# Kernel tuning notes

Hardware: AMD Instinct MI355X
Metric: run time of the kernel (lower is better)

The kernel has to match this reference:

```python
import jax, jax.numpy as jnp
import numpy as np

DIM = 192
HEADS = 6
WIN = (2, 6, 2)
N_TOK = WIN[0] * WIN[1] * WIN[2]  # 24
MLP_HID = 4 * DIM


def _rel_pos_index():
    wh, ww, wd = WIN
    ch, cw, cd = np.meshgrid(np.arange(wh), np.arange(ww), np.arange(wd), indexing='ij')
    coords = np.stack([ch, cw, cd]).reshape(3, -1)  # (3, N)
    rel = coords[:, :, None] - coords[:, None, :]   # (3, N, N)
    rel = rel.transpose(1, 2, 0).copy()
    rel[:, :, 0] += wh - 1
    rel[:, :, 1] += ww - 1
    rel[:, :, 2] += wd - 1
    rel[:, :, 0] *= (2 * ww - 1) * (2 * wd - 1)
    rel[:, :, 1] *= 2 * wd - 1
    return rel.sum(-1)  # (N, N) int


def setup_inputs() -> dict:
    key = jax.random.key(0)
    ks = jax.random.split(key, 8)
    wh, ww, wd = WIN
    table_len = (2 * wh - 1) * (2 * ww - 1) * (2 * wd - 1)
    return {
        'x': jax.random.normal(ks[0], (2, 48, 96, 14, DIM), jnp.float32),
        'ln1_g': jnp.ones((DIM,), jnp.float32),
        'ln1_b': jnp.zeros((DIM,), jnp.float32),
        'qkv_w': jax.random.normal(ks[1], (DIM, 3 * DIM), jnp.float32) * 0.02,  # [in, out]
        'qkv_b': jnp.zeros((3 * DIM,), jnp.float32),
        'bias_table': jax.random.normal(ks[2], (table_len, HEADS), jnp.float32) * 0.02,
        'proj_w': jax.random.normal(ks[3], (DIM, DIM), jnp.float32) * 0.02,
        'proj_b': jnp.zeros((DIM,), jnp.float32),
        'ln2_g': jnp.ones((DIM,), jnp.float32),
        'ln2_b': jnp.zeros((DIM,), jnp.float32),
        'mlp_w1': jax.random.normal(ks[4], (DIM, MLP_HID), jnp.float32) * 0.02,
        'mlp_b1': jnp.zeros((MLP_HID,), jnp.float32),
        'mlp_w2': jax.random.normal(ks[5], (MLP_HID, DIM), jnp.float32) * 0.02,
        'mlp_b2': jnp.zeros((DIM,), jnp.float32),
        'rel_index': jnp.asarray(_rel_pos_index(), jnp.int32),  # (N, N)
    }


def _layernorm(x, g, b, eps=1e-5):
    mu = jnp.mean(x, -1, keepdims=True)
    var = jnp.mean(jnp.square(x - mu), -1, keepdims=True)
    return (x - mu) * jax.lax.rsqrt(var + eps) * g + b


def reference(x, ln1_g, ln1_b, qkv_w, qkv_b, bias_table, proj_w, proj_b,
              ln2_g, ln2_b, mlp_w1, mlp_b1, mlp_w2, mlp_b2, rel_index):
    B, H, W, D, C = x.shape
    wh, ww, wd = WIN
    pad_h, pad_w, pad_d = (-H) % wh, (-W) % ww, (-D) % wd
    if pad_h or pad_w or pad_d:
        x = jnp.pad(x, ((0, 0), (0, pad_h), (0, pad_w), (0, pad_d), (0, 0)))
    Hp, Wp, Dp = H + pad_h, W + pad_w, D + pad_d
    # window partition -> (num_windows*B, N, C)
    xw = x.reshape(B, Hp // wh, wh, Wp // ww, ww, Dp // wd, wd, C)
    xw = xw.transpose(0, 1, 3, 5, 2, 4, 6, 7).reshape(-1, N_TOK, C)
    shortcut = xw

    h = _layernorm(xw, ln1_g, ln1_b)
    qkv = (h @ qkv_w + qkv_b).reshape(-1, N_TOK, 3, HEADS, C // HEADS)
    q, k, v = qkv[:, :, 0], qkv[:, :, 1], qkv[:, :, 2]  # (Bw, N, H, hd)
    scale = (C // HEADS) ** -0.5
    attn = jnp.einsum('bnhd,bmhd->bhnm', q * scale, k)
    bias = bias_table[rel_index]  # (N, N, HEADS)
    attn = attn + bias.transpose(2, 0, 1)[None]
    attn = jax.nn.softmax(attn, axis=-1)
    out = jnp.einsum('bhnm,bmhd->bnhd', attn, v).reshape(-1, N_TOK, C)
    out = out @ proj_w + proj_b
    xw = shortcut + out

    h2 = _layernorm(xw, ln2_g, ln2_b)
    mlp = jax.nn.gelu(h2 @ mlp_w1 + mlp_b1, approximate=False) @ mlp_w2 + mlp_b2
    xw = xw + mlp

    # reverse window partition
    xw = xw.reshape(B, Hp // wh, Wp // ww, Dp // wd, wh, ww, wd, C)
    xw = xw.transpose(0, 1, 4, 2, 5, 3, 6, 7).reshape(B, Hp, Wp, Dp, C)
    if pad_h or pad_w or pad_d:
        xw = xw[:, :H, :W, :D, :]
    return xw
```

## Files before the change

### kernel.cpp

```cpp
#include <hip/hip_runtime.h>
#include <hip/hip_bf16.h>
#include <math.h>

typedef __bf16 bf16_t;
typedef __bf16 bf16x8 __attribute__((ext_vector_type(8)));
typedef float  f32x4  __attribute__((ext_vector_type(4)));

#define NBLK 2688
#define WP_QKV  0
#define WP_PROJ 55296
#define WP_MLP1 73728
#define WP_MLP2 147456
#define WP_TOT  221184
#define WF_QKV  0
#define WF_PROJ 110592
#define WF_MLP1 147456
#define WF_MLP2 294912

__global__ void preproc_all(const float* __restrict__ qkv_w, const float* __restrict__ proj_w,
                            const float* __restrict__ mlp_w1, const float* __restrict__ mlp_w2,
                            bf16_t* __restrict__ dst) {
    int p = blockIdx.x * 256 + threadIdx.x;
    if (p >= WP_TOT) return;
    const float* W; int N, Kt; int q = p;
    if (p < WP_PROJ)      { W = qkv_w;  N = 576; Kt = 6;  }
    else if (p < WP_MLP1) { W = proj_w; N = 192; Kt = 6;  q -= WP_PROJ; }
    else if (p < WP_MLP2) { W = mlp_w1; N = 768; Kt = 6;  q -= WP_MLP1; }
    else                  { W = mlp_w2; N = 192; Kt = 24; q -= WP_MLP2; }
    int j    = (q & 3) * 2;
    int lane = (q >> 2) & 63;
    int kt   = (q >> 8) % Kt;
    int nt   = (q >> 8) / Kt;
    int k = kt * 32 + (lane >> 4) * 8 + j;
    int n = nt * 16 + (lane & 15);
    union { bf16_t h[2]; unsigned u; } pk;
    pk.h[0] = (bf16_t)W[k * N + n];
    pk.h[1] = (bf16_t)W[(k + 1) * N + n];
    *(unsigned*)(dst + p * 2) = pk.u;
}

__global__ __launch_bounds__(384, 3)
void pangu_main(const float* __restrict__ x,
                const float* __restrict__ ln1_g, const float* __restrict__ ln1_b,
                const float* __restrict__ qkv_b,
                const float* __restrict__ bias_table,
                const float* __restrict__ proj_b,
                const float* __restrict__ ln2_g, const float* __restrict__ ln2_b,
                const float* __restrict__ mlp_b1, const float* __restrict__ mlp_b2,
                const int* __restrict__ rel_index,
                const bf16_t* __restrict__ wf,
                float* __restrict__ out)
{
    __shared__ __align__(16) unsigned char arena[115200];
    __shared__ int   sRowOff[48];
    __shared__ float sMu[48], sRs[48];

    unsigned char* aAb   = arena;
    unsigned char* aOb   = arena;
    unsigned char* aH2b  = arena;
    unsigned char* xw2b  = arena + 19200;
    unsigned char* aHidb = arena + 38400;
    bf16_t* aO   = (bf16_t*)aOb;
    bf16_t* aHid = (bf16_t*)aHidb;
    bf16_t* xw2h = (bf16_t*)xw2b;

    const int t    = threadIdx.x;
    const int lane = t & 63;
    const int wv   = t >> 6;
    const int quad = lane >> 4;
    const int l15  = lane & 15;
    const int q4   = quad * 4;

    if (t < 48) {
        int win = t / 24, tok = t % 24;
        int W = blockIdx.x * 2 + win;
        int id_ = W % 7;  int r1 = W / 7;
        int iw_ = r1 % 16; int r2 = r1 / 16;
        int ih_ = r2 % 24; int b  = r2 / 24;
        int i = tok / 12, j = (tok % 12) / 2, k = tok % 2;
        sRowOff[t] = (((b * 48 + ih_ * 2 + i) * 96 + iw_ * 6 + j) * 14 + id_ * 2 + k) * 192;
    }
    __syncthreads();

    {
        int r48 = t >> 3, l = t & 7;
        const float* xr = x + sRowOff[r48];
        float4 v[6];
        #pragma unroll
        for (int s = 0; s < 6; ++s) v[s] = *(const float4*)(xr + l * 4 + s * 32);
        float sm = 0.f, s2 = 0.f;
        #pragma unroll
        for (int s = 0; s < 6; ++s) {
            sm += v[s].x + v[s].y + v[s].z + v[s].w;
            s2 += v[s].x * v[s].x + v[s].y * v[s].y + v[s].z * v[s].z + v[s].w * v[s].w;
        }
        sm += __shfl_xor(sm, 1); s2 += __shfl_xor(s2, 1);
        sm += __shfl_xor(sm, 2); s2 += __shfl_xor(s2, 2);
        sm += __shfl_xor(sm, 4); s2 += __shfl_xor(s2, 4);
        float mu = sm * (1.f / 192.f);
        float var = s2 * (1.f / 192.f) - mu * mu;
        float rs = rsqrtf(var + 1e-5f);
        int row = r48;
        #pragma unroll
        for (int s = 0; s < 6; ++s) {
            int c = l * 4 + s * 32;
            union { bf16_t h[4]; uint2 u; } pk;
            pk.h[0] = (bf16_t)((v[s].x - mu) * rs * ln1_g[c]     + ln1_b[c]);
            pk.h[1] = (bf16_t)((v[s].y - mu) * rs * ln1_g[c + 1] + ln1_b[c + 1]);
            pk.h[2] = (bf16_t)((v[s].z - mu) * rs * ln1_g[c + 2] + ln1_b[c + 2]);
            pk.h[3] = (bf16_t)((v[s].w - mu) * rs * ln1_g[c + 3] + ln1_b[c + 3]);
            *(uint2*)(aAb + row * 400 + c * 2) = pk.u;
        }
    }
    __syncthreads();

    {
        const int h = wv;
        unsigned char* wb = arena + 19200 + wv * 9344;
        bf16_t* Qb  = (bf16_t*)wb;
        bf16_t* Kb2 = (bf16_t*)(wb + 1920);
        bf16_t* Vt  = (bf16_t*)(wb + 5760);
        bf16_t* Pb  = (bf16_t*)wb;

        {
            f32x4 acc[3][4];
            const int ntg[4] = {12+2*h, 13+2*h, 24+2*h, 25+2*h};
            float bq[4];
            #pragma unroll
            for (int n = 0; n < 4; ++n) bq[n] = qkv_b[ntg[n] * 16 + l15];
            #pragma unroll
            for (int m = 0; m < 3; ++m)
                #pragma unroll
                for (int n = 0; n < 4; ++n)
                    acc[m][n] = (f32x4){bq[n], bq[n], bq[n], bq[n]};
            for (int kt = 0; kt < 6; ++kt) {
                bf16x8 af[3];
                #pragma unroll
                for (int m = 0; m < 3; ++m)
                    af[m] = *(const bf16x8*)(aAb + (l15 + m * 16) * 400 + kt * 64 + quad * 16);
                #pragma unroll
                for (int n = 0; n < 4; ++n) {
                    bf16x8 bfr = *(const bf16x8*)(wf + WF_QKV + ((ntg[n] * 6 + kt) * 64 + lane) * 8);
                    #pragma unroll
                    for (int m = 0; m < 3; ++m)
                        acc[m][n] = __builtin_amdgcn_mfma_f32_16x16x32_bf16(af[m], bfr, acc[m][n], 0, 0, 0);
                }
            }
            #pragma unroll
            for (int m = 0; m < 3; ++m)
                #pragma unroll
                for (int i = 0; i < 4; ++i) {
                    int row = m * 16 + q4 + i;
                    #pragma unroll
                    for (int nt = 0; nt < 2; ++nt) {
                        int d = nt * 16 + l15;
                        Kb2[row * 40 + d] = (bf16_t)(acc[m][nt][i]);
                        Vt[d * 56 + row]  = (bf16_t)(acc[m][2+nt][i]);
                    }
                }
            {
                int d = lane >> 1, half = lane & 1;
                *(uint2*)((unsigned char*)Vt + d * 112 + 96 + half * 8) = make_uint2(0u, 0u);
            }
        }

        f32x4 qacc[3][2];
        {
            const int ntg[2] = {2*h, 2*h+1};
            float bq[2];
            #pragma unroll
            for (int n = 0; n < 2; ++n) bq[n] = qkv_b[ntg[n] * 16 + l15];
            #pragma unroll
            for (int m = 0; m < 3; ++m)
                #pragma unroll
                for (int n = 0; n < 2; ++n)
                    qacc[m][n] = (f32x4){bq[n], bq[n], bq[n], bq[n]};
            for (int kt = 0; kt < 6; ++kt) {
                bf16x8 af[3];
                #pragma unroll
                for (int m = 0; m < 3; ++m)
                    af[m] = *(const bf16x8*)(aAb + (l15 + m * 16) * 400 + kt * 64 + quad * 16);
                #pragma unroll
                for (int n = 0; n < 2; ++n) {
                    bf16x8 bfr = *(const bf16x8*)(wf + WF_QKV + ((ntg[n] * 6 + kt) * 64 + lane) * 8);
                    #pragma unroll
                    for (int m = 0; m < 3; ++m)
                        qacc[m][n] = __builtin_amdgcn_mfma_f32_16x16x32_bf16(af[m], bfr, qacc[m][n], 0, 0, 0);
                }
            }
        }
        __syncthreads();

        const float scale = 0.1767766952966369f;
        #pragma unroll
        for (int win = 0; win < 2; ++win) {
            #pragma unroll
            for (int m = 0; m < 3; ++m)
                #pragma unroll
                for (int i = 0; i < 4; ++i) {
                    int tok = m * 16 + q4 + i - win * 24;
                    if (tok >= 0 && tok < 24) {
                        #pragma unroll
                        for (int nt = 0; nt < 2; ++nt)
                            Qb[tok * 40 + nt * 16 + l15] = (bf16_t)(qacc[m][nt][i] * scale);
                    }
                }
            f32x4 sacc[2][2];
            #pragma unroll
            for (int mt = 0; mt < 2; ++mt)
                #pragma unroll
                for (int nt = 0; nt < 2; ++nt)
                    #pragma unroll
                    for (int i = 0; i < 4; ++i) {
                        int n = mt * 16 + q4 + i; if (n > 23) n = 23;
                        int m = nt * 16 + l15;    if (m > 23) m = 23;
                        sacc[mt][nt][i] = bias_table[rel_index[n * 24 + m] * 6 + h];
                    }
            #pragma unroll
            for (int nt = 0; nt < 2; ++nt) {
                bf16x8 kf = *(const bf16x8*)((unsigned char*)Kb2 + (win * 24 + l15 + nt * 16) * 80 + quad * 16);
                #pragma unroll
                for (int mt = 0; mt < 2; ++mt) {
                    bf16x8 qf = *(const bf16x8*)((unsigned char*)Qb + (l15 + mt * 16) * 80 + quad * 16);
                    sacc[mt][nt] = __builtin_amdgcn_mfma_f32_16x16x32_bf16(qf, kf, sacc[mt][nt], 0, 0, 0);
                }
            }
            #pragma unroll
            for (int mt = 0; mt < 2; ++mt)
                #pragma unroll
                for (int i = 0; i < 4; ++i) {
                    float s0 = sacc[mt][0][i];
                    float s1m = (l15 < 8) ? sacc[mt][1][i] : -1e30f;
                    float mx = fmaxf(s0, s1m);
                    mx = fmaxf(mx, __shfl_xor(mx, 1));
                    mx = fmaxf(mx, __shfl_xor(mx, 2));
                    mx = fmaxf(mx, __shfl_xor(mx, 4));
                    mx = fmaxf(mx, __shfl_xor(mx, 8));
                    float e0 = __expf(s0 - mx);
                    float e1 = (l15 < 8) ? __expf(sacc[mt][1][i] - mx) : 0.f;
                    float sum = e0 + e1;
                    sum += __shfl_xor(sum, 1);
                    sum += __shfl_xor(sum, 2);
                    sum += __shfl_xor(sum, 4);
                    sum += __shfl_xor(sum, 8);
                    float inv = 1.f / sum;
                    sacc[mt][0][i] = e0 * inv;
                    sacc[mt][1][i] = e1 * inv;
                }
            #pragma unroll
            for (int mt = 0; mt < 2; ++mt)
                #pragma unroll
                for (int i = 0; i < 4; ++i) {
                    int r = mt * 16 + q4 + i;
                    if (r < 24) {
                        Pb[r * 40 + l15]      = (bf16_t)sacc[mt][0][i];
                        Pb[r * 40 + 16 + l15] = (bf16_t)sacc[mt][1][i];
                    }
                }
            f32x4 oacc[2][2];
            #pragma unroll
            for (int mt = 0; mt < 2; ++mt)
                #pragma unroll
                for (int nt = 0; nt < 2; ++nt)
                    oacc[mt][nt] = (f32x4){0.f, 0.f, 0.f, 0.f};
            #pragma unroll
            for (int nt = 0; nt < 2; ++nt) {
                bf16x8 vf = *(const bf16x8*)((unsigned char*)Vt + (l15 + nt * 16) * 112 + win * 48 + quad * 16);
                #pragma unroll
                for (int mt = 0; mt < 2; ++mt) {
                    bf16x8 pf = *(const bf16x8*)((unsigned char*)Pb + (l15 + mt * 16) * 80 + quad * 16);
                    oacc[mt][nt] = __builtin_amdgcn_mfma_f32_16x16x32_bf16(pf, vf, oacc[mt][nt], 0, 0, 0);
                }
            }
            #pragma unroll
            for (int mt = 0; mt < 2; ++mt)
                #pragma unroll
                for (int i = 0; i < 4; ++i) {
                    int tok = mt * 16 + q4 + i;
                    if (tok < 24) {
                        int r = win * 24 + tok;
                        #pragma unroll
                        for (int nt = 0; nt < 2; ++nt)
                            aO[r * 200 + h * 32 + nt * 16 + l15] = (bf16_t)oacc[mt][nt][i];
                    }
                }
        }
    }
    __syncthreads();

    float rxw[3][2][4];
    {
        f32x4 pacc[3][2];
        #pragma unroll
        for (int m = 0; m < 3; ++m)
            #pragma unroll
            for (int n = 0; n < 2; ++n) pacc[m][n] = (f32x4){0.f, 0.f, 0.f, 0.f};
        for (int kt = 0; kt < 6; ++kt) {
            bf16x8 af[3];
            #pragma unroll
            for (int m = 0; m < 3; ++m)
                af[m] = *(const bf16x8*)(aOb + (l15 + m * 16) * 400 + kt * 64 + quad * 16);
            #pragma unroll
            for (int n = 0; n < 2; ++n) {
                int NT = wv * 2 + n;
                bf16x8 bfr = *(const bf16x8*)(wf + WF_PROJ + ((NT * 6 + kt) * 64 + lane) * 8);
                #pragma unroll
                for (int m = 0; m < 3; ++m)
                    pacc[m][n] = __builtin_amdgcn_mfma_f32_16x16x32_bf16(af[m], bfr, pacc[m][n], 0, 0, 0);
            }
        }
        __syncthreads();
        #pragma unroll
        for (int n = 0; n < 2; ++n) {
            int c = (wv * 2 + n) * 16 + l15;
            float pb = proj_b[c];
            #pragma unroll
            for (int m = 0; m < 3; ++m)
                #pragma unroll
                for (int i = 0; i < 4; ++i) {
                    int r = m * 16 + q4 + i;
                    float val = x[sRowOff[r] + c] + pb + pacc[m][n][i];
                    rxw[m][n][i] = val;
                    xw2h[r * 200 + c] = (bf16_t)val;
                }
        }
    }
    __syncthreads();

    {
        int r = t >> 3, l = t & 7;
        float sm = 0.f, s2 = 0.f;
        #pragma unroll
        for (int s = 0; s < 6; ++s) {
            union { bf16_t h[4]; uint2 u; } pk;
            pk.u = *(const uint2*)(xw2b + r * 400 + l * 8 + s * 64);
            #pragma unroll
            for (int z = 0; z < 4; ++z) { float v = (float)pk.h[z]; sm += v; s2 += v * v; }
        }
        sm += __shfl_xor(sm, 1); s2 += __shfl_xor(s2, 1);
        sm += __shfl_xor(sm, 2); s2 += __shfl_xor(s2, 2);
        sm += __shfl_xor(sm, 4); s2 += __shfl_xor(s2, 4);
        if (l == 0) {
            float mu = sm * (1.f / 192.f);
            float var = s2 * (1.f / 192.f) - mu * mu;
            sMu[r] = mu; sRs[r] = rsqrtf(var + 1e-5f);
        }
    }
    __syncthreads();
    for (int p = t; p < 4608; p += 384) {
        int r = p / 96, c2 = p % 96, c = c2 * 2;
        float mu = sMu[r], rs = sRs[r];
        union { bf16_t h[2]; unsigned u; } in, pk;
        in.u = *(const unsigned*)(xw2b + r * 400 + c2 * 4);
        pk.h[0] = (bf16_t)(((float)in.h[0] - mu) * rs * ln2_g[c]     + ln2_b[c]);
        pk.h[1] = (bf16_t)(((float)in.h[1] - mu) * rs * ln2_g[c + 1] + ln2_b[c + 1]);
        *(unsigned*)(aH2b + r * 400 + c2 * 4) = pk.u;
    }
    __syncthreads();

    f32x4 acc2[3][2];
    #pragma unroll
    for (int m = 0; m < 3; ++m)
        #pragma unroll
        for (int n = 0; n < 2; ++n) {
            float b2 = mlp_b2[(wv * 2 + n) * 16 + l15];
            acc2[m][n] = (f32x4){b2, b2, b2, b2};
        }
    for (int ch = 0; ch < 4; ++ch) {
        f32x4 a1[3][2];
        #pragma unroll
        for (int m = 0; m < 3; ++m)
            #pragma unroll
            for (int n = 0; n < 2; ++n) {
                float b1 = mlp_b1[ch * 192 + (wv * 2 + n) * 16 + l15];
                a1[m][n] = (f32x4){b1, b1, b1, b1};
            }
        for (int kt = 0; kt < 6; ++kt) {
            bf16x8 af[3];
            #pragma unroll
            for (int m = 0; m < 3; ++m)
                af[m] = *(const bf16x8*)(aH2b + (l15 + m * 16) * 400 + kt * 64 + quad * 16);
            #pragma unroll
            for (int n = 0; n < 2; ++n) {
                int NT = ch * 12 + wv * 2 + n;
                bf16x8 bfr = *(const bf16x8*)(wf + WF_MLP1 + ((NT * 6 + kt) * 64 + lane) * 8);
                #pragma unroll
                for (int m = 0; m < 3; ++m)
                    a1[m][n] = __builtin_amdgcn_mfma_f32_16x16x32_bf16(af[m], bfr, a1[m][n], 0, 0, 0);
            }
        }
        #pragma unroll
        for (int n = 0; n < 2; ++n) {
            int c = ch * 192 + (wv * 2 + n) * 16 + l15;
            #pragma unroll
            for (int m = 0; m < 3; ++m)
                #pragma unroll
                for (int i = 0; i < 4; ++i) {
                    int r = m * 16 + q4 + i;
                    float v = a1[m][n][i];
                    float g = 0.5f * v * (1.f + erff(v * 0.70710678118654752f));
                    aHid[r * 800 + c] = (bf16_t)g;
                }
        }
    }
    __syncthreads();
    for (int ktg = 0; ktg < 24; ++ktg) {
        bf16x8 af[3];
        #pragma unroll
        for (int m = 0; m < 3; ++m)
            af[m] = *(const bf16x8*)(aHidb + (l15 + m * 16) * 1600 + ktg * 64 + quad * 16);
        #pragma unroll
        for (int n = 0; n < 2; ++n) {
            int NT = wv * 2 + n;
            bf16x8 bfr = *(const bf16x8*)(wf + WF_MLP2 + ((NT * 24 + ktg) * 64 + lane) * 8);
            #pragma unroll
            for (int m = 0; m < 3; ++m)
                acc2[m][n] = __builtin_amdgcn_mfma_f32_16x16x32_bf16(af[m], bfr, acc2[m][n], 0, 0, 0);
        }
    }

    #pragma unroll
    for (int n = 0; n < 2; ++n) {
        int c = (wv * 2 + n) * 16 + l15;
        #pragma unroll
        for (int m = 0; m < 3; ++m)
            #pragma unroll
            for (int i = 0; i < 4; ++i) {
                int r = m * 16 + q4 + i;
                out[sRowOff[r] + c] = rxw[m][n][i] + acc2[m][n][i];
            }
    }
}

extern "C" void kernel_launch(void* const* d_in, const int* in_sizes, int n_in,
                              void* d_out, int out_size, void* d_ws, size_t ws_size,
                              hipStream_t stream) {
    const float* x          = (const float*)d_in[0];
    const float* ln1_g      = (const float*)d_in[1];
    const float* ln1_b      = (const float*)d_in[2];
    const float* qkv_w      = (const float*)d_in[3];
    const float* qkv_b      = (const float*)d_in[4];
    const float* bias_table = (const float*)d_in[5];
    const float* proj_w     = (const float*)d_in[6];
    const float* proj_b     = (const float*)d_in[7];
    const float* ln2_g      = (const float*)d_in[8];
    const float* ln2_b      = (const float*)d_in[9];
    const float* mlp_w1     = (const float*)d_in[10];
    const float* mlp_b1     = (const float*)d_in[11];
    const float* mlp_w2     = (const float*)d_in[12];
    const float* mlp_b2     = (const float*)d_in[13];
    const int*   rel_index  = (const int*)d_in[14];
    float* out = (float*)d_out;
    bf16_t* wsb = (bf16_t*)d_ws;

    preproc_all<<<(WP_TOT + 255) / 256, 256, 0, stream>>>(qkv_w, proj_w, mlp_w1, mlp_w2, wsb);

    pangu_main<<<NBLK, 384, 0, stream>>>(
        x, ln1_g, ln1_b, qkv_b, bias_table, proj_b, ln2_g, ln2_b,
        mlp_b1, mlp_b2, rel_index, wsb, out);
}
```

Baseline: 505.1 us.

## Process four windows per 768-thread block with two row groups per head

Each block now handles four windows (96 tokens) with 12 waves. Waves are paired per head, and each wave covers half the token rows, so every bf16 weight fragment fetched from global memory serves twice as many rows. The MLP hidden layer is split into two 384-wide chunks, with the second matmul accumulating after each chunk, which shrinks the hidden buffer enough for the larger tile to fit in LDS. The cost is about 152KB of shared memory per block, which allows only one block per CU, plus an extra barrier in the MLP loop.

```diff
diff --git a/kernel.cpp b/kernel.cpp
--- a/kernel.cpp
+++ b/kernel.cpp
@@ -6,7 +6,7 @@
 typedef __bf16 bf16x8 __attribute__((ext_vector_type(8)));
 typedef float  f32x4  __attribute__((ext_vector_type(4)));
 
-#define NBLK 2688
+#define NBLK 1344
 #define WP_QKV  0
 #define WP_PROJ 55296
 #define WP_MLP1 73728
@@ -39,7 +39,7 @@
     *(unsigned*)(dst + p * 2) = pk.u;
 }
 
-__global__ __launch_bounds__(384, 3)
+__global__ __launch_bounds__(768, 3)
 void pangu_main(const float* __restrict__ x,
                 const float* __restrict__ ln1_g, const float* __restrict__ ln1_b,
                 const float* __restrict__ qkv_b,
@@ -51,15 +51,15 @@
                 const bf16_t* __restrict__ wf,
                 float* __restrict__ out)
 {
-    __shared__ __align__(16) unsigned char arena[115200];
-    __shared__ int   sRowOff[48];
-    __shared__ float sMu[48], sRs[48];
+    __shared__ __align__(16) unsigned char arena[152064];
+    __shared__ int   sRowOff[96];
+    __shared__ float sMu[96], sRs[96];
 
     unsigned char* aAb   = arena;
     unsigned char* aOb   = arena;
     unsigned char* aH2b  = arena;
-    unsigned char* xw2b  = arena + 19200;
-    unsigned char* aHidb = arena + 38400;
+    unsigned char* xw2b  = arena + 38400;
+    unsigned char* aHidb = arena + 76800;
     bf16_t* aO   = (bf16_t*)aOb;
     bf16_t* aHid = (bf16_t*)aHidb;
     bf16_t* xw2h = (bf16_t*)xw2b;
@@ -67,13 +67,15 @@
     const int t    = threadIdx.x;
     const int lane = t & 63;
     const int wv   = t >> 6;
+    const int h    = wv >> 1;
+    const int g    = wv & 1;
     const int quad = lane >> 4;
     const int l15  = lane & 15;
     const int q4   = quad * 4;
 
-    if (t < 48) {
+    if (t < 96) {
         int win = t / 24, tok = t % 24;
-        int W = blockIdx.x * 2 + win;
+        int W = blockIdx.x * 4 + win;
         int id_ = W % 7;  int r1 = W / 7;
         int iw_ = r1 % 16; int r2 = r1 / 16;
         int ih_ = r2 % 24; int b  = r2 / 24;
@@ -83,8 +85,8 @@
     __syncthreads();
 
     {
-        int r48 = t >> 3, l = t & 7;
-        const float* xr = x + sRowOff[r48];
+        int r96 = t >> 3, l = t & 7;
+        const float* xr = x + sRowOff[r96];
         float4 v[6];
         #pragma unroll
         for (int s = 0; s < 6; ++s) v[s] = *(const float4*)(xr + l * 4 + s * 32);
@@ -100,23 +102,21 @@
         float mu = sm * (1.f / 192.f);
         float var = s2 * (1.f / 192.f) - mu * mu;
         float rs = rsqrtf(var + 1e-5f);
-        int row = r48;
         #pragma unroll
         for (int s = 0; s < 6; ++s) {
             int c = l * 4 + s * 32;
-            union { bf16_t h[4]; uint2 u; } pk;
-            pk.h[0] = (bf16_t)((v[s].x - mu) * rs * ln1_g[c]     + ln1_b[c]);
-            pk.h[1] = (bf16_t)((v[s].y - mu) * rs * ln1_g[c + 1] + ln1_b[c + 1]);
-            pk.h[2] = (bf16_t)((v[s].z - mu) * rs * ln1_g[c + 2] + ln1_b[c + 2]);
-            pk.h[3] = (bf16_t)((v[s].w - mu) * rs * ln1_g[c + 3] + ln1_b[c + 3]);
-            *(uint2*)(aAb + row * 400 + c * 2) = pk.u;
+            union { bf16_t h4[4]; uint2 u; } pk;
+            pk.h4[0] = (bf16_t)((v[s].x - mu) * rs * ln1_g[c]     + ln1_b[c]);
+            pk.h4[1] = (bf16_t)((v[s].y - mu) * rs * ln1_g[c + 1] + ln1_b[c + 1]);
+            pk.h4[2] = (bf16_t)((v[s].z - mu) * rs * ln1_g[c + 2] + ln1_b[c + 2]);
+            pk.h4[3] = (bf16_t)((v[s].w - mu) * rs * ln1_g[c + 3] + ln1_b[c + 3]);
+            *(uint2*)(aAb + r96 * 400 + c * 2) = pk.u;
         }
     }
     __syncthreads();
 
     {
-        const int h = wv;
-        unsigned char* wb = arena + 19200 + wv * 9344;
+        unsigned char* wb = arena + 38400 + wv * 9344;
         bf16_t* Qb  = (bf16_t*)wb;
         bf16_t* Kb2 = (bf16_t*)(wb + 1920);
         bf16_t* Vt  = (bf16_t*)(wb + 5760);
@@ -137,7 +137,7 @@
                 bf16x8 af[3];
                 #pragma unroll
                 for (int m = 0; m < 3; ++m)
-                    af[m] = *(const bf16x8*)(aAb + (l15 + m * 16) * 400 + kt * 64 + quad * 16);
+                    af[m] = *(const bf16x8*)(aAb + (l15 + (3*g + m) * 16) * 400 + kt * 64 + quad * 16);
                 #pragma unroll
                 for (int n = 0; n < 4; ++n) {
                     bf16x8 bfr = *(const bf16x8*)(wf + WF_QKV + ((ntg[n] * 6 + kt) * 64 + lane) * 8);
@@ -179,7 +179,7 @@
                 bf16x8 af[3];
                 #pragma unroll
                 for (int m = 0; m < 3; ++m)
-                    af[m] = *(const bf16x8*)(aAb + (l15 + m * 16) * 400 + kt * 64 + quad * 16);
+                    af[m] = *(const bf16x8*)(aAb + (l15 + (3*g + m) * 16) * 400 + kt * 64 + quad * 16);
                 #pragma unroll
                 for (int n = 0; n < 2; ++n) {
                     bf16x8 bfr = *(const bf16x8*)(wf + WF_QKV + ((ntg[n] * 6 + kt) * 64 + lane) * 8);
@@ -193,12 +193,12 @@
 
         const float scale = 0.1767766952966369f;
         #pragma unroll
-        for (int win = 0; win < 2; ++win) {
-            #pragma unroll
-            for (int m = 0; m < 3; ++m)
-                #pragma unroll
-                for (int i = 0; i < 4; ++i) {
-                    int tok = m * 16 + q4 + i - win * 24;
+        for (int w01 = 0; w01 < 2; ++w01) {
+            #pragma unroll
+            for (int m = 0; m < 3; ++m)
+                #pragma unroll
+                for (int i = 0; i < 4; ++i) {
+                    int tok = m * 16 + q4 + i - w01 * 24;
                     if (tok >= 0 && tok < 24) {
                         #pragma unroll
                         for (int nt = 0; nt < 2; ++nt)
@@ -218,7 +218,7 @@
                     }
             #pragma unroll
             for (int nt = 0; nt < 2; ++nt) {
-                bf16x8 kf = *(const bf16x8*)((unsigned char*)Kb2 + (win * 24 + l15 + nt * 16) * 80 + quad * 16);
+                bf16x8 kf = *(const bf16x8*)((unsigned char*)Kb2 + (w01 * 24 + l15 + nt * 16) * 80 + quad * 16);
                 #pragma unroll
                 for (int mt = 0; mt < 2; ++mt) {
                     bf16x8 qf = *(const bf16x8*)((unsigned char*)Qb + (l15 + mt * 16) * 80 + quad * 16);
@@ -265,7 +265,7 @@
                     oacc[mt][nt] = (f32x4){0.f, 0.f, 0.f, 0.f};
             #pragma unroll
             for (int nt = 0; nt < 2; ++nt) {
-                bf16x8 vf = *(const bf16x8*)((unsigned char*)Vt + (l15 + nt * 16) * 112 + win * 48 + quad * 16);
+                bf16x8 vf = *(const bf16x8*)((unsigned char*)Vt + (l15 + nt * 16) * 112 + w01 * 48 + quad * 16);
                 #pragma unroll
                 for (int mt = 0; mt < 2; ++mt) {
                     bf16x8 pf = *(const bf16x8*)((unsigned char*)Pb + (l15 + mt * 16) * 80 + quad * 16);
@@ -278,7 +278,7 @@
                 for (int i = 0; i < 4; ++i) {
                     int tok = mt * 16 + q4 + i;
                     if (tok < 24) {
-                        int r = win * 24 + tok;
+                        int r = 48 * g + w01 * 24 + tok;
                         #pragma unroll
                         for (int nt = 0; nt < 2; ++nt)
                             aO[r * 200 + h * 32 + nt * 16 + l15] = (bf16_t)oacc[mt][nt][i];
@@ -299,26 +299,25 @@
             bf16x8 af[3];
             #pragma unroll
             for (int m = 0; m < 3; ++m)
-                af[m] = *(const bf16x8*)(aOb + (l15 + m * 16) * 400 + kt * 64 + quad * 16);
+                af[m] = *(const bf16x8*)(aOb + (l15 + (3*g + m) * 16) * 400 + kt * 64 + quad * 16);
             #pragma unroll
             for (int n = 0; n < 2; ++n) {
-                int NT = wv * 2 + n;
+                int NT = 2 * h + n;
                 bf16x8 bfr = *(const bf16x8*)(wf + WF_PROJ + ((NT * 6 + kt) * 64 + lane) * 8);
                 #pragma unroll
                 for (int m = 0; m < 3; ++m)
                     pacc[m][n] = __builtin_amdgcn_mfma_f32_16x16x32_bf16(af[m], bfr, pacc[m][n], 0, 0, 0);
             }
         }
-        __syncthreads();
         #pragma unroll
         for (int n = 0; n < 2; ++n) {
-            int c = (wv * 2 + n) * 16 + l15;
+            int c = (2 * h + n) * 16 + l15;
             float pb = proj_b[c];
             #pragma unroll
             for (int m = 0; m < 3; ++m)
                 #pragma unroll
                 for (int i = 0; i < 4; ++i) {
-                    int r = m * 16 + q4 + i;
+                    int r = (3*g + m) * 16 + q4 + i;
                     float val = x[sRowOff[r] + c] + pb + pacc[m][n][i];
                     rxw[m][n][i] = val;
                     xw2h[r * 200 + c] = (bf16_t)val;
@@ -332,10 +331,10 @@
         float sm = 0.f, s2 = 0.f;
         #pragma unroll
         for (int s = 0; s < 6; ++s) {
-            union { bf16_t h[4]; uint2 u; } pk;
+            union { bf16_t h4[4]; uint2 u; } pk;
             pk.u = *(const uint2*)(xw2b + r * 400 + l * 8 + s * 64);
             #pragma unroll
-            for (int z = 0; z < 4; ++z) { float v = (float)pk.h[z]; sm += v; s2 += v * v; }
+            for (int z = 0; z < 4; ++z) { float v = (float)pk.h4[z]; sm += v; s2 += v * v; }
         }
         sm += __shfl_xor(sm, 1); s2 += __shfl_xor(s2, 1);
         sm += __shfl_xor(sm, 2); s2 += __shfl_xor(s2, 2);
@@ -347,13 +346,13 @@
         }
     }
     __syncthreads();
-    for (int p = t; p < 4608; p += 384) {
+    for (int p = t; p < 9216; p += 768) {
         int r = p / 96, c2 = p % 96, c = c2 * 2;
         float mu = sMu[r], rs = sRs[r];
-        union { bf16_t h[2]; unsigned u; } in, pk;
+        union { bf16_t h2[2]; unsigned u; } in, pk;
         in.u = *(const unsigned*)(xw2b + r * 400 + c2 * 4);
-        pk.h[0] = (bf16_t)(((float)in.h[0] - mu) * rs * ln2_g[c]     + ln2_b[c]);
-        pk.h[1] = (bf16_t)(((float)in.h[1] - mu) * rs * ln2_g[c + 1] + ln2_b[c + 1]);
+        pk.h2[0] = (bf16_t)(((float)in.h2[0] - mu) * rs * ln2_g[c]     + ln2_b[c]);
+        pk.h2[1] = (bf16_t)(((float)in.h2[1] - mu) * rs * ln2_g[c + 1] + ln2_b[c + 1]);
         *(unsigned*)(aH2b + r * 400 + c2 * 4) = pk.u;
     }
     __syncthreads();
@@ -363,26 +362,26 @@
     for (int m = 0; m < 3; ++m)
         #pragma unroll
         for (int n = 0; n < 2; ++n) {
-            float b2 = mlp_b2[(wv * 2 + n) * 16 + l15];
+            float b2 = mlp_b2[(2 * h + n) * 16 + l15];
             acc2[m][n] = (f32x4){b2, b2, b2, b2};
         }
-    for (int ch = 0; ch < 4; ++ch) {
-        f32x4 a1[3][2];
+    for (int ch = 0; ch < 2; ++ch) {
+        f32x4 a1[3][4];
         #pragma unroll
         for (int m = 0; m < 3; ++m)
             #pragma unroll
-            for (int n = 0; n < 2; ++n) {
-                float b1 = mlp_b1[ch * 192 + (wv * 2 + n) * 16 + l15];
+            for (int n = 0; n < 4; ++n) {
+                float b1 = mlp_b1[(ch * 24 + 4 * h + n) * 16 + l15];
                 a1[m][n] = (f32x4){b1, b1, b1, b1};
             }
         for (int kt = 0; kt < 6; ++kt) {
             bf16x8 af[3];
             #pragma unroll
             for (int m = 0; m < 3; ++m)
-                af[m] = *(const bf16x8*)(aH2b + (l15 + m * 16) * 400 + kt * 64 + quad * 16);
-            #pragma unroll
-            for (int n = 0; n < 2; ++n) {
-                int NT = ch * 12 + wv * 2 + n;
+                af[m] = *(const bf16x8*)(aH2b + (l15 + (3*g + m) * 16) * 400 + kt * 64 + quad * 16);
+            #pragma unroll
+            for (int n = 0; n < 4; ++n) {
+                int NT = ch * 24 + 4 * h + n;
                 bf16x8 bfr = *(const bf16x8*)(wf + WF_MLP1 + ((NT * 6 + kt) * 64 + lane) * 8);
                 #pragma unroll
                 for (int m = 0; m < 3; ++m)
@@ -390,43 +389,45 @@
             }
         }
         #pragma unroll
-        for (int n = 0; n < 2; ++n) {
-            int c = ch * 192 + (wv * 2 + n) * 16 + l15;
-            #pragma unroll
-            for (int m = 0; m < 3; ++m)
-                #pragma unroll
-                for (int i = 0; i < 4; ++i) {
-                    int r = m * 16 + q4 + i;
+        for (int n = 0; n < 4; ++n) {
+            int c = (4 * h + n) * 16 + l15;
+            #pragma unroll
+            for (int m = 0; m < 3; ++m)
+                #pragma unroll
+                for (int i = 0; i < 4; ++i) {
+                    int r = (3*g + m) * 16 + q4 + i;
                     float v = a1[m][n][i];
-                    float g = 0.5f * v * (1.f + erff(v * 0.70710678118654752f));
-                    aHid[r * 800 + c] = (bf16_t)g;
-                }
-        }
-    }
-    __syncthreads();
-    for (int ktg = 0; ktg < 24; ++ktg) {
-        bf16x8 af[3];
-        #pragma unroll
-        for (int m = 0; m < 3; ++m)
-            af[m] = *(const bf16x8*)(aHidb + (l15 + m * 16) * 1600 + ktg * 64 + quad * 16);
-        #pragma unroll
-        for (int n = 0; n < 2; ++n) {
-            int NT = wv * 2 + n;
-            bf16x8 bfr = *(const bf16x8*)(wf + WF_MLP2 + ((NT * 24 + ktg) * 64 + lane) * 8);
-            #pragma unroll
-            for (int m = 0; m < 3; ++m)
-                acc2[m][n] = __builtin_amdgcn_mfma_f32_16x16x32_bf16(af[m], bfr, acc2[m][n], 0, 0, 0);
-        }
+                    float gl = 0.5f * v * (1.f + erff(v * 0.70710678118654752f));
+                    aHid[r * 392 + c] = (bf16_t)gl;
+                }
+        }
+        __syncthreads();
+        for (int ktl = 0; ktl < 12; ++ktl) {
+            bf16x8 af[3];
+            #pragma unroll
+            for (int m = 0; m < 3; ++m)
+                af[m] = *(const bf16x8*)(aHidb + (l15 + (3*g + m) * 16) * 784 + ktl * 64 + quad * 16);
+            #pragma unroll
+            for (int n = 0; n < 2; ++n) {
+                int NT = 2 * h + n;
+                int ktg = ch * 12 + ktl;
+                bf16x8 bfr = *(const bf16x8*)(wf + WF_MLP2 + ((NT * 24 + ktg) * 64 + lane) * 8);
+                #pragma unroll
+                for (int m = 0; m < 3; ++m)
+                    acc2[m][n] = __builtin_amdgcn_mfma_f32_16x16x32_bf16(af[m], bfr, acc2[m][n], 0, 0, 0);
+            }
+        }
+        if (ch == 0) __syncthreads();
     }
 
     #pragma unroll
     for (int n = 0; n < 2; ++n) {
-        int c = (wv * 2 + n) * 16 + l15;
+        int c = (2 * h + n) * 16 + l15;
         #pragma unroll
         for (int m = 0; m < 3; ++m)
             #pragma unroll
             for (int i = 0; i < 4; ++i) {
-                int r = m * 16 + q4 + i;
+                int r = (3*g + m) * 16 + q4 + i;
                 out[sRowOff[r] + c] = rxw[m][n][i] + acc2[m][n][i];
             }
     }
@@ -455,7 +456,7 @@
 
     preproc_all<<<(WP_TOT + 255) / 256, 256, 0, stream>>>(qkv_w, proj_w, mlp_w1, mlp_w2, wsb);
 
-    pangu_main<<<NBLK, 384, 0, stream>>>(
+    pangu_main<<<NBLK, 768, 0, stream>>>(
         x, ln1_g, ln1_b, qkv_b, bias_table, proj_b, ln2_g, ln2_b,
         mlp_b1, mlp_b2, rel_index, wsb, out);
 }
```

Result: faster. 473.6 us (-6.2%).
